# Optimization experiments

Hardware: AMD Instinct MI355X
Metric: run time of the kernel (lower is better)

Reference implementation:

```python
import jax, jax.numpy as jnp
import numpy as np
from jax import lax

# Module dims (match init_kwargs / input_specs)
CIN, COUT, K, STRIDE = 8, 16, 3, 2
U = V = 32                      # input spatial size (inshape = (CIN, U, V))
UO = VO = U // STRIDE           # 'same' padding with stride -> 16
IN_DIM = CIN * U * V + 1        # 8193 (homogeneous)
OUT_DIM = COUT * UO * VO + 1    # 4097 (homogeneous)
N = 1024                        # batch (columns of x_affine)


def setup_inputs() -> dict:
    key = jax.random.key(0)
    k1, k2, k3, k4, k5 = jax.random.split(key, 5)
    w = jax.random.normal(k1, (COUT, CIN, K, K), dtype=jnp.float32) * 0.1
    b = jax.random.normal(k2, (COUT,), dtype=jnp.float32) * 0.1
    # Keying matrices (dense stand-ins for the sparse keys); scaled to keep values sane.
    A = jax.random.normal(k3, (OUT_DIM, OUT_DIM), dtype=jnp.float32) / np.sqrt(OUT_DIM)
    Ainv = jax.random.normal(k4, (IN_DIM, IN_DIM), dtype=jnp.float32) / np.sqrt(IN_DIM)
    x_affine = jax.random.normal(k5, (IN_DIM, N), dtype=jnp.float32)
    return {"w": w, "b": b, "A": A, "Ainv": Ainv, "x_affine": x_affine}


def _toeplitz_conv_apply(z, w, b):
    """Apply the affine Toeplitz conv matrix T to z of shape (CIN*U*V+1, N).
    T = [[conv, bias], [0, 1]] so T@z = [conv(z[:-1]) + b*z[-1]; z[-1]]."""
    n = z.shape[1]
    hom = z[-1]                                   # (N,) homogeneous row
    x = z[:-1].T.reshape(n, CIN, U, V)            # (N, CIN, U, V)
    y = lax.conv_general_dilated(
        x, w, window_strides=(STRIDE, STRIDE), padding="SAME",
        dimension_numbers=("NCHW", "OIHW", "NCHW"))  # (N, COUT, UO, VO)
    y = y + b[None, :, None, None] * hom[:, None, None, None]
    yf = y.reshape(n, COUT * UO * VO).T           # (COUT*UO*VO, N)
    return jnp.concatenate([yf, hom[None, :]], axis=0)  # (OUT_DIM, N)


def reference(w, b, A, Ainv, x_affine):
    # What @ x = A @ T @ Ainv @ x  (factored; never materializes What)
    z = Ainv @ x_affine                # (IN_DIM, N)
    t = _toeplitz_conv_apply(z, w, b)  # (OUT_DIM, N)
    return A @ t                       # (OUT_DIM, N)
```

## Files before the change

kernel.cpp:

```cpp
#include <hip/hip_runtime.h>

#define IN_DIM 8193
#define OUT_DIM 4097
#define NB 1024
#define MP1 8448
#define KP1 8256
#define MP2 4352
#define KP2 4160

typedef __attribute__((ext_vector_type(8))) short short8;
typedef __attribute__((ext_vector_type(4))) float f32x4;

__device__ __forceinline__ unsigned short f2bf(float f) {
  unsigned int u = __float_as_uint(f);
  u = (u + 0x7fffu + ((u >> 16) & 1u)) >> 16;
  return (unsigned short)u;
}

__global__ __launch_bounds__(256) void cvt_pad_kernel(
    const float* __restrict__ src, unsigned short* __restrict__ dst,
    int sR, int sC, int dR, int dC) {
  int gid = blockIdx.x * 256 + threadIdx.x;
  int i4 = gid * 4;
  if (i4 >= dR * dC) return;
  int r = i4 / dC;
  int c = i4 - r * dC;
  unsigned short o[4];
#pragma unroll
  for (int j = 0; j < 4; ++j) {
    int cc = c + j;
    float v = (r < sR && cc < sC) ? src[(size_t)r * sC + cc] : 0.f;
    o[j] = f2bf(v);
  }
  unsigned int lo = (unsigned)o[0] | ((unsigned)o[1] << 16);
  unsigned int hi = (unsigned)o[2] | ((unsigned)o[3] << 16);
  *reinterpret_cast<uint2*>(dst + i4) = make_uint2(lo, hi);
}

__global__ __launch_bounds__(256) void transpose_cvt_kernel(
    const float* __restrict__ src, unsigned short* __restrict__ dst,
    int K, int N, int Kp) {
  __shared__ float tl[32][33];
  const int ntk = Kp >> 5;
  int bx = blockIdx.x % ntk;
  int by = blockIdx.x / ntk;
  int k0 = bx * 32, n0 = by * 32;
  int tx = threadIdx.x & 31, ty = threadIdx.x >> 5;
#pragma unroll
  for (int i = 0; i < 4; ++i) {
    int k = k0 + ty + i * 8;
    tl[ty + i * 8][tx] = (k < K) ? src[(size_t)k * N + n0 + tx] : 0.f;
  }
  __syncthreads();
#pragma unroll
  for (int i = 0; i < 4; ++i) {
    int n = n0 + ty + i * 8;
    dst[(size_t)n * Kp + k0 + tx] = f2bf(tl[tx][ty + i * 8]);
  }
}

__global__ __launch_bounds__(256) void zero_kernel(float4* __restrict__ p, int n) {
  int i = blockIdx.x * 256 + threadIdx.x;
  if (i < n) p[i] = make_float4(0.f, 0.f, 0.f, 0.f);
}

template <int NKT>
__global__ __launch_bounds__(512) void gemm_sk(
    const unsigned short* __restrict__ Ab,
    const unsigned short* __restrict__ Bt,
    float* __restrict__ C,
    int Kp, int Mout, int total_units) {
  extern __shared__ unsigned short lds[];
  const int tid = threadIdx.x;
  const int wid = tid >> 6;
  const int lane = tid & 63;
  const int wm = (wid >> 2) << 7;
  const int wn = (wid & 3) << 6;
  const int b = blockIdx.x;
  const int bw = ((b & 7) << 5) | (b >> 3);
  const int s = (int)(((long long)bw * total_units) >> 8);
  const int e = (int)(((long long)(bw + 1) * total_units) >> 8);

  const int g0 = ((lane >> 4) ^ (lane & 7)) * 8;
  const int g1 = ((4 + (lane >> 4)) ^ (lane & 7)) * 8;
  const int alo = (lane & 15) * 64;
  const int bhalf = (wn >> 7) << 1;
  const int ahalf = (wid >> 2) << 1;
  const int bsub = ((wn & 64) << 6) + alo;

#define STAGE(UNIT, ISA)                                                       \
  do {                                                                         \
    const int rq_ = (UNIT);                                                    \
    const int us_ = rq_ < e - 1 ? rq_ : e - 1;                                 \
    const int par_ = rq_ & 1;                                                  \
    const int tau_ = us_ / NKT;                                                \
    const int kt_ = us_ - tau_ * NKT;                                          \
    const size_t gr_ = (size_t)((ISA) ? (tau_ >> 2) : (tau_ & 3)) << 8;        \
    const unsigned short* M_ = (ISA) ? Ab : Bt;                                \
    _Pragma("unroll")                                                          \
    for (int h_ = 0; h_ < 2; ++h_) {                                           \
      _Pragma("unroll")                                                        \
      for (int L_ = 0; L_ < 2; ++L_) {                                         \
        const int s_ = L_ * 512 + tid;                                         \
        const int row_ = s_ >> 3;                                              \
        const int gl_ = (s_ & 7) ^ (row_ & 7);                                 \
        const unsigned short* g_ = M_ + (gr_ + (h_ << 7) + row_) * (size_t)Kp  \
                                      + (kt_ << 6) + gl_ * 8;                  \
        unsigned short* l_ = lds + (((ISA) ? 0 : 4) + (h_ << 1) + par_) * 8192 \
                                 + (size_t)(L_ * 512 + wid * 64) * 8;          \
        __builtin_amdgcn_global_load_lds(                                      \
            (const __attribute__((address_space(1))) void*)g_,                 \
            (__attribute__((address_space(3))) void*)l_, 16, 0, 0);            \
      }                                                                        \
    }                                                                          \
  } while (0)

#define MFMA16(BV0, BV1, NF0, NF1)                                             \
  do {                                                                         \
    __builtin_amdgcn_s_setprio(1);                                             \
    _Pragma("unroll")                                                          \
    for (int mf_ = 0; mf_ < 8; ++mf_) {                                        \
      asm volatile("v_mfma_f32_16x16x32_bf16 %0, %1, %2, %0"                   \
                   : "+v"(acc[mf_][NF0]) : "v"(af[mf_]), "v"(BV0));            \
      asm volatile("v_mfma_f32_16x16x32_bf16 %0, %1, %2, %0"                   \
                   : "+v"(acc[mf_][NF1]) : "v"(af[mf_]), "v"(BV1));            \
    }                                                                          \
    __builtin_amdgcn_s_setprio(0);                                             \
  } while (0)

#define FLUSH(TAU)                                                             \
  do {                                                                         \
    const int bm_ = (TAU) >> 2, bn_ = (TAU) & 3;                               \
    _Pragma("unroll")                                                          \
    for (int mf_ = 0; mf_ < 8; ++mf_) {                                        \
      const int rb_ = (bm_ << 8) + wm + mf_ * 16 + ((lane >> 4) << 2);         \
      _Pragma("unroll")                                                        \
      for (int nf_ = 0; nf_ < 4; ++nf_) {                                      \
        const int col_ = (bn_ << 8) + wn + nf_ * 16 + (lane & 15);             \
        _Pragma("unroll")                                                      \
        for (int r_ = 0; r_ < 4; ++r_) {                                       \
          const int row_ = rb_ + r_;                                           \
          if (row_ < Mout)                                                     \
            unsafeAtomicAdd(&C[(size_t)row_ * NB + col_], acc[mf_][nf_][r_]);  \
        }                                                                      \
        acc[mf_][nf_] = (f32x4)(0.0f);                                         \
      }                                                                        \
    }                                                                          \
  } while (0)

  f32x4 acc[8][4];
#pragma unroll
  for (int i = 0; i < 8; ++i)
#pragma unroll
    for (int j = 0; j < 4; ++j) acc[i][j] = (f32x4)(0.0f);

  STAGE(s, 1);
  STAGE(s, 0);
  STAGE(s + 1, 1);

  int tau_cur = s / NKT;
  for (int u = s; u < e; ++u) {
    const int par = u & 1;
    const unsigned short* Ab_ = lds + (ahalf + par) * 8192 + alo;
    const unsigned short* Bb_ = lds + (4 + bhalf + par) * 8192 + bsub;
    short8 af[8], b0, b1;
    __builtin_amdgcn_sched_barrier(0);
    asm volatile("s_waitcnt vmcnt(4)" ::: "memory");
    __builtin_amdgcn_s_barrier();
    __builtin_amdgcn_sched_barrier(0);
    STAGE(u + 1, 0);
#pragma unroll
    for (int mf = 0; mf < 8; ++mf)
      af[mf] = *reinterpret_cast<const short8*>(Ab_ + mf * 1024 + g0);
    b0 = *reinterpret_cast<const short8*>(Bb_ + 0 * 1024 + g0);
    b1 = *reinterpret_cast<const short8*>(Bb_ + 1 * 1024 + g0);
    MFMA16(b0, b1, 0, 1);
    b0 = *reinterpret_cast<const short8*>(Bb_ + 2 * 1024 + g0);
    b1 = *reinterpret_cast<const short8*>(Bb_ + 3 * 1024 + g0);
    MFMA16(b0, b1, 2, 3);
#pragma unroll
    for (int mf = 0; mf < 8; ++mf)
      af[mf] = *reinterpret_cast<const short8*>(Ab_ + mf * 1024 + g1);
    b0 = *reinterpret_cast<const short8*>(Bb_ + 2 * 1024 + g1);
    b1 = *reinterpret_cast<const short8*>(Bb_ + 3 * 1024 + g1);
    MFMA16(b0, b1, 2, 3);
    __builtin_amdgcn_sched_barrier(0);
    __builtin_amdgcn_s_barrier();
    __builtin_amdgcn_sched_barrier(0);
    STAGE(u + 2, 1);
    b0 = *reinterpret_cast<const short8*>(Bb_ + 0 * 1024 + g1);
    b1 = *reinterpret_cast<const short8*>(Bb_ + 1 * 1024 + g1);
    MFMA16(b0, b1, 0, 1);
    if (u + 1 >= e) {
      FLUSH(tau_cur);
    } else {
      const int tn = (u + 1) / NKT;
      if (tn != tau_cur) { FLUSH(tau_cur); tau_cur = tn; }
    }
  }
#undef STAGE
#undef MFMA16
#undef FLUSH
}

__global__ __launch_bounds__(256) void conv_tT_kernel(
    const float* __restrict__ z, const float* __restrict__ w,
    const float* __restrict__ bias, unsigned short* __restrict__ tT) {
  const int gid = blockIdx.x * 256 + threadIdx.x;
  const int n = gid & 1023;
  const int rg = gid >> 10;
  const int r0 = rg << 3;
  const float hom = z[(size_t)8192 * 1024 + n];
  unsigned short o[8];
  if (r0 >= 4096) {
#pragma unroll
    for (int j = 0; j < 8; ++j) o[j] = f2bf((r0 + j == 4096) ? hom : 0.f);
  } else {
    const int co = r0 >> 8;
    const int uo = (r0 >> 4) & 15;
    const int vo0 = r0 & 15;
    float acc[8];
    const float bb = bias[co];
#pragma unroll
    for (int j = 0; j < 8; ++j) acc[j] = bb * hom;
    for (int ci = 0; ci < 8; ++ci) {
#pragma unroll
      for (int kh = 0; kh < 3; ++kh) {
        const int u = uo * 2 + kh;
        if (u >= 32) continue;
        const float* zbase = z + (size_t)(ci * 1024 + u * 32) * 1024 + n;
#pragma unroll
        for (int kw = 0; kw < 3; ++kw) {
          const float wv = w[((co * 8 + ci) * 3 + kh) * 3 + kw];
#pragma unroll
          for (int j = 0; j < 8; ++j) {
            const int v = (vo0 + j) * 2 + kw;
            if (v < 32) acc[j] += wv * zbase[(size_t)v * 1024];
          }
        }
      }
    }
#pragma unroll
    for (int j = 0; j < 8; ++j) o[j] = f2bf(acc[j]);
  }
  uint4 pv;
  pv.x = (unsigned)o[0] | ((unsigned)o[1] << 16);
  pv.y = (unsigned)o[2] | ((unsigned)o[3] << 16);
  pv.z = (unsigned)o[4] | ((unsigned)o[5] << 16);
  pv.w = (unsigned)o[6] | ((unsigned)o[7] << 16);
  *reinterpret_cast<uint4*>(tT + (size_t)n * KP2 + r0) = pv;
}

extern "C" void kernel_launch(void* const* d_in, const int* in_sizes, int n_in,
                              void* d_out, int out_size, void* d_ws, size_t ws_size,
                              hipStream_t stream) {
  const float* w    = (const float*)d_in[0];
  const float* bias = (const float*)d_in[1];
  const float* A    = (const float*)d_in[2];
  const float* Ainv = (const float*)d_in[3];
  const float* x    = (const float*)d_in[4];
  float* out = (float*)d_out;

  char* ws = (char*)d_ws;
  unsigned short* Ainv_b = (unsigned short*)ws;
  unsigned short* xT_b   = (unsigned short*)(ws + (size_t)MP1 * KP1 * 2);
  float*          z      = (float*)(ws + (size_t)MP1 * KP1 * 2 + (size_t)NB * KP1 * 2);
  unsigned short* tT_b   = (unsigned short*)(ws + (size_t)MP1 * KP1 * 2 + (size_t)NB * KP1 * 2
                                             + (size_t)MP1 * NB * 4);
  unsigned short* A2_b   = Ainv_b;
  (void)ws_size; (void)in_sizes; (void)n_in; (void)out_size;

  hipFuncSetAttribute((const void*)gemm_sk<129>,
                      hipFuncAttributeMaxDynamicSharedMemorySize, 131072);
  hipFuncSetAttribute((const void*)gemm_sk<65>,
                      hipFuncAttributeMaxDynamicSharedMemorySize, 131072);

  cvt_pad_kernel<<<(MP1 * KP1 / 4 + 255) / 256, 256, 0, stream>>>(
      Ainv, Ainv_b, IN_DIM, IN_DIM, MP1, KP1);
  transpose_cvt_kernel<<<(KP1 / 32) * (NB / 32), 256, 0, stream>>>(
      x, xT_b, IN_DIM, NB, KP1);
  zero_kernel<<<(MP1 * NB / 4 + 255) / 256, 256, 0, stream>>>(
      (float4*)z, MP1 * NB / 4);
  gemm_sk<129><<<256, 512, 131072, stream>>>(
      Ainv_b, xT_b, z, KP1, MP1, 33 * 4 * 129);
  conv_tT_kernel<<<(520 * 1024) / 256, 256, 0, stream>>>(z, w, bias, tT_b);
  cvt_pad_kernel<<<(MP2 * KP2 / 4 + 255) / 256, 256, 0, stream>>>(
      A, A2_b, OUT_DIM, OUT_DIM, MP2, KP2);
  zero_kernel<<<(OUT_DIM * NB / 4 + 255) / 256, 256, 0, stream>>>(
      (float4*)out, OUT_DIM * NB / 4);
  gemm_sk<65><<<256, 512, 131072, stream>>>(
      A2_b, tT_b, out, KP2, OUT_DIM, 17 * 4 * 65);
}
```

Measured before the change: 439.8 us.

## Replace stream-K atomic GEMMs with fixed split-K partial buffers plus reductions

Both GEMMs move from stream-K scheduling with atomic flushes to a fixed data-parallel tiling over the unpadded 8192/4096 rows, with a static K split into separate partial buffers. The partials are reduced afterwards: the first GEMM's two halves are summed inside the conv kernel, and the second GEMM's four halves by a new sum kernel. The odd homogeneous rows are handled apart: the z row is a dot product fused into the transpose kernel, and the last output row comes from a small GEMV kernel. This removes the atomics, the zeroing passes and the padded-row work, at the cost of extra partial-buffer traffic and fp32 reduction passes.

```diff
diff --git a/kernel.cpp b/kernel.cpp
--- a/kernel.cpp
+++ b/kernel.cpp
@@ -3,9 +3,9 @@
 #define IN_DIM 8193
 #define OUT_DIM 4097
 #define NB 1024
-#define MP1 8448
+#define M1 8192
 #define KP1 8256
-#define MP2 4352
+#define M2 4096
 #define KP2 4160
 
 typedef __attribute__((ext_vector_type(8))) short short8;
@@ -15,6 +15,9 @@
   unsigned int u = __float_as_uint(f);
   u = (u + 0x7fffu + ((u >> 16) & 1u)) >> 16;
   return (unsigned short)u;
+}
+__device__ __forceinline__ float bf2f(unsigned short u) {
+  return __uint_as_float(((unsigned int)u) << 16);
 }
 
 __global__ __launch_bounds__(256) void cvt_pad_kernel(
@@ -37,8 +40,9 @@
   *reinterpret_cast<uint2*>(dst + i4) = make_uint2(lo, hi);
 }
 
-__global__ __launch_bounds__(256) void transpose_cvt_kernel(
+__global__ __launch_bounds__(256) void transpose_cvt_zh_kernel(
     const float* __restrict__ src, unsigned short* __restrict__ dst,
+    const float* __restrict__ arow, float* __restrict__ zh,
     int K, int N, int Kp) {
   __shared__ float tl[32][33];
   const int ntk = Kp >> 5;
@@ -51,11 +55,17 @@
     int k = k0 + ty + i * 8;
     tl[ty + i * 8][tx] = (k < K) ? src[(size_t)k * N + n0 + tx] : 0.f;
   }
+  const float av = (k0 + tx < K) ? arow[k0 + tx] : 0.f;
   __syncthreads();
 #pragma unroll
   for (int i = 0; i < 4; ++i) {
     int n = n0 + ty + i * 8;
-    dst[(size_t)n * Kp + k0 + tx] = f2bf(tl[tx][ty + i * 8]);
+    float v = tl[tx][ty + i * 8];
+    dst[(size_t)n * Kp + k0 + tx] = f2bf(v);
+    float c = av * v;
+#pragma unroll
+    for (int m = 1; m <= 16; m <<= 1) c += __shfl_xor(c, m);
+    if (tx == 0) atomicAdd(&zh[n], c);
   }
 }
 
@@ -64,22 +74,27 @@
   if (i < n) p[i] = make_float4(0.f, 0.f, 0.f, 0.f);
 }
 
-template <int NKT>
-__global__ __launch_bounds__(512) void gemm_sk(
+template <int NKT, int NSPLIT, int BMBITS, int MROWS>
+__global__ __launch_bounds__(512) void gemm_dp(
     const unsigned short* __restrict__ Ab,
     const unsigned short* __restrict__ Bt,
-    float* __restrict__ C,
-    int Kp, int Mout, int total_units) {
+    float* __restrict__ C, int Kp) {
   extern __shared__ unsigned short lds[];
   const int tid = threadIdx.x;
   const int wid = tid >> 6;
   const int lane = tid & 63;
+  const int b = blockIdx.x;
+  const int x = b & 7, q = b >> 3;
+  const int bm = (q & ((1 << BMBITS) - 1)) * 8 + x;
+  const int bn = (q >> BMBITS) & 3;
+  const int sp = q >> (BMBITS + 2);
   const int wm = (wid >> 2) << 7;
   const int wn = (wid & 3) << 6;
-  const int b = blockIdx.x;
-  const int bw = ((b & 7) << 5) | (b >> 3);
-  const int s = (int)(((long long)bw * total_units) >> 8);
-  const int e = (int)(((long long)(bw + 1) * total_units) >> 8);
+
+  const int qk = NKT / NSPLIT, rrk = NKT % NSPLIT;
+  const int kt0 = sp * qk + (sp < rrk ? sp : rrk);
+  const int T = qk + (sp < rrk ? 1 : 0);
+  float* Cp = C + (size_t)sp * MROWS * NB;
 
   const int g0 = ((lane >> 4) ^ (lane & 7)) * 8;
   const int g1 = ((4 + (lane >> 4)) ^ (lane & 7)) * 8;
@@ -88,15 +103,13 @@
   const int ahalf = (wid >> 2) << 1;
   const int bsub = ((wn & 64) << 6) + alo;
 
-#define STAGE(UNIT, ISA)                                                       \
+#define STAGE(TT, ISA)                                                         \
   do {                                                                         \
-    const int rq_ = (UNIT);                                                    \
-    const int us_ = rq_ < e - 1 ? rq_ : e - 1;                                 \
-    const int par_ = rq_ & 1;                                                  \
-    const int tau_ = us_ / NKT;                                                \
-    const int kt_ = us_ - tau_ * NKT;                                          \
-    const size_t gr_ = (size_t)((ISA) ? (tau_ >> 2) : (tau_ & 3)) << 8;        \
+    const int tt_ = (TT);                                                      \
+    const int kc_ = kt0 + (tt_ < T - 1 ? tt_ : T - 1);                         \
+    const int par_ = tt_ & 1;                                                  \
     const unsigned short* M_ = (ISA) ? Ab : Bt;                                \
+    const int br_ = ((ISA) ? bm : bn) << 8;                                    \
     _Pragma("unroll")                                                          \
     for (int h_ = 0; h_ < 2; ++h_) {                                           \
       _Pragma("unroll")                                                        \
@@ -104,8 +117,8 @@
         const int s_ = L_ * 512 + tid;                                         \
         const int row_ = s_ >> 3;                                              \
         const int gl_ = (s_ & 7) ^ (row_ & 7);                                 \
-        const unsigned short* g_ = M_ + (gr_ + (h_ << 7) + row_) * (size_t)Kp  \
-                                      + (kt_ << 6) + gl_ * 8;                  \
+        const unsigned short* g_ = M_ + (size_t)(br_ + (h_ << 7) + row_) * Kp  \
+                                      + (kc_ << 6) + gl_ * 8;                  \
         unsigned short* l_ = lds + (((ISA) ? 0 : 4) + (h_ << 1) + par_) * 8192 \
                                  + (size_t)(L_ * 512 + wid * 64) * 8;          \
         __builtin_amdgcn_global_load_lds(                                      \
@@ -128,39 +141,18 @@
     __builtin_amdgcn_s_setprio(0);                                             \
   } while (0)
 
-#define FLUSH(TAU)                                                             \
-  do {                                                                         \
-    const int bm_ = (TAU) >> 2, bn_ = (TAU) & 3;                               \
-    _Pragma("unroll")                                                          \
-    for (int mf_ = 0; mf_ < 8; ++mf_) {                                        \
-      const int rb_ = (bm_ << 8) + wm + mf_ * 16 + ((lane >> 4) << 2);         \
-      _Pragma("unroll")                                                        \
-      for (int nf_ = 0; nf_ < 4; ++nf_) {                                      \
-        const int col_ = (bn_ << 8) + wn + nf_ * 16 + (lane & 15);             \
-        _Pragma("unroll")                                                      \
-        for (int r_ = 0; r_ < 4; ++r_) {                                       \
-          const int row_ = rb_ + r_;                                           \
-          if (row_ < Mout)                                                     \
-            unsafeAtomicAdd(&C[(size_t)row_ * NB + col_], acc[mf_][nf_][r_]);  \
-        }                                                                      \
-        acc[mf_][nf_] = (f32x4)(0.0f);                                         \
-      }                                                                        \
-    }                                                                          \
-  } while (0)
-
   f32x4 acc[8][4];
 #pragma unroll
   for (int i = 0; i < 8; ++i)
 #pragma unroll
     for (int j = 0; j < 4; ++j) acc[i][j] = (f32x4)(0.0f);
 
-  STAGE(s, 1);
-  STAGE(s, 0);
-  STAGE(s + 1, 1);
-
-  int tau_cur = s / NKT;
-  for (int u = s; u < e; ++u) {
-    const int par = u & 1;
+  STAGE(0, 1);
+  STAGE(0, 0);
+  STAGE(1, 1);
+
+  for (int t = 0; t < T; ++t) {
+    const int par = t & 1;
     const unsigned short* Ab_ = lds + (ahalf + par) * 8192 + alo;
     const unsigned short* Bb_ = lds + (4 + bhalf + par) * 8192 + bsub;
     short8 af[8], b0, b1;
@@ -168,7 +160,7 @@
     asm volatile("s_waitcnt vmcnt(4)" ::: "memory");
     __builtin_amdgcn_s_barrier();
     __builtin_amdgcn_sched_barrier(0);
-    STAGE(u + 1, 0);
+    STAGE(t + 1, 0);
 #pragma unroll
     for (int mf = 0; mf < 8; ++mf)
       af[mf] = *reinterpret_cast<const short8*>(Ab_ + mf * 1024 + g0);
@@ -187,30 +179,36 @@
     __builtin_amdgcn_sched_barrier(0);
     __builtin_amdgcn_s_barrier();
     __builtin_amdgcn_sched_barrier(0);
-    STAGE(u + 2, 1);
+    STAGE(t + 2, 1);
     b0 = *reinterpret_cast<const short8*>(Bb_ + 0 * 1024 + g1);
     b1 = *reinterpret_cast<const short8*>(Bb_ + 1 * 1024 + g1);
     MFMA16(b0, b1, 0, 1);
-    if (u + 1 >= e) {
-      FLUSH(tau_cur);
-    } else {
-      const int tn = (u + 1) / NKT;
-      if (tn != tau_cur) { FLUSH(tau_cur); tau_cur = tn; }
-    }
   }
 #undef STAGE
 #undef MFMA16
-#undef FLUSH
+
+#pragma unroll
+  for (int mf = 0; mf < 8; ++mf) {
+    const int rb = (bm << 8) + wm + mf * 16 + ((lane >> 4) << 2);
+#pragma unroll
+    for (int nf = 0; nf < 4; ++nf) {
+      const int col = (bn << 8) + wn + nf * 16 + (lane & 15);
+#pragma unroll
+      for (int r = 0; r < 4; ++r)
+        Cp[(size_t)(rb + r) * NB + col] = acc[mf][nf][r];
+    }
+  }
 }
 
 __global__ __launch_bounds__(256) void conv_tT_kernel(
-    const float* __restrict__ z, const float* __restrict__ w,
+    const float* __restrict__ za, const float* __restrict__ zb,
+    const float* __restrict__ zh, const float* __restrict__ w,
     const float* __restrict__ bias, unsigned short* __restrict__ tT) {
   const int gid = blockIdx.x * 256 + threadIdx.x;
   const int n = gid & 1023;
   const int rg = gid >> 10;
   const int r0 = rg << 3;
-  const float hom = z[(size_t)8192 * 1024 + n];
+  const float hom = zh[n];
   unsigned short o[8];
   if (r0 >= 4096) {
 #pragma unroll
@@ -228,14 +226,17 @@
       for (int kh = 0; kh < 3; ++kh) {
         const int u = uo * 2 + kh;
         if (u >= 32) continue;
-        const float* zbase = z + (size_t)(ci * 1024 + u * 32) * 1024 + n;
+        const size_t zoff = (size_t)(ci * 1024 + u * 32) * 1024 + n;
 #pragma unroll
         for (int kw = 0; kw < 3; ++kw) {
           const float wv = w[((co * 8 + ci) * 3 + kh) * 3 + kw];
 #pragma unroll
           for (int j = 0; j < 8; ++j) {
             const int v = (vo0 + j) * 2 + kw;
-            if (v < 32) acc[j] += wv * zbase[(size_t)v * 1024];
+            if (v < 32) {
+              const size_t e = zoff + (size_t)v * 1024;
+              acc[j] += wv * (za[e] + zb[e]);
+            }
           }
         }
       }
@@ -249,6 +250,47 @@
   pv.z = (unsigned)o[4] | ((unsigned)o[5] << 16);
   pv.w = (unsigned)o[6] | ((unsigned)o[7] << 16);
   *reinterpret_cast<uint4*>(tT + (size_t)n * KP2 + r0) = pv;
+}
+
+__global__ __launch_bounds__(256) void sum4_kernel(
+    const float* __restrict__ p, float* __restrict__ out, int n4) {
+  const int i = blockIdx.x * 256 + threadIdx.x;
+  if (i >= n4) return;
+  const size_t stride4 = (size_t)M2 * NB / 4;
+  const float4* p4 = (const float4*)p;
+  float4 a = p4[i];
+  float4 b = p4[i + stride4];
+  float4 c = p4[i + 2 * stride4];
+  float4 d = p4[i + 3 * stride4];
+  float4 r;
+  r.x = (a.x + b.x) + (c.x + d.x);
+  r.y = (a.y + b.y) + (c.y + d.y);
+  r.z = (a.z + b.z) + (c.z + d.z);
+  r.w = (a.w + b.w) + (c.w + d.w);
+  reinterpret_cast<float4*>(out)[i] = r;
+}
+
+__global__ __launch_bounds__(256) void outrow_kernel(
+    const unsigned short* __restrict__ A2row,
+    const unsigned short* __restrict__ tT, float* __restrict__ out) {
+  const int wid = threadIdx.x >> 6, lane = threadIdx.x & 63;
+  const int n = blockIdx.x * 4 + wid;
+  const unsigned short* trow = tT + (size_t)n * KP2;
+  float acc = 0.f;
+#pragma unroll
+  for (int it = 0; it < 9; ++it) {
+    const int i8 = it * 64 + lane;
+    if (i8 < KP2 / 8) {
+      short8 tv = *reinterpret_cast<const short8*>(trow + i8 * 8);
+      short8 av = *reinterpret_cast<const short8*>(A2row + i8 * 8);
+#pragma unroll
+      for (int j = 0; j < 8; ++j)
+        acc += bf2f((unsigned short)tv[j]) * bf2f((unsigned short)av[j]);
+    }
+  }
+#pragma unroll
+  for (int m = 1; m <= 32; m <<= 1) acc += __shfl_xor(acc, m);
+  if (lane == 0) out[(size_t)4096 * NB + n] = acc;
 }
 
 extern "C" void kernel_launch(void* const* d_in, const int* in_sizes, int n_in,
@@ -262,32 +304,39 @@
   float* out = (float*)d_out;
 
   char* ws = (char*)d_ws;
+  const size_t o_xT = (size_t)M1 * KP1 * 2;
+  const size_t o_z2 = o_xT + (size_t)NB * KP1 * 2;
+  const size_t o_tT = o_z2 + (size_t)2 * M1 * NB * 4;
+  const size_t o_zh = o_tT + (size_t)NB * KP2 * 2;
   unsigned short* Ainv_b = (unsigned short*)ws;
-  unsigned short* xT_b   = (unsigned short*)(ws + (size_t)MP1 * KP1 * 2);
-  float*          z      = (float*)(ws + (size_t)MP1 * KP1 * 2 + (size_t)NB * KP1 * 2);
-  unsigned short* tT_b   = (unsigned short*)(ws + (size_t)MP1 * KP1 * 2 + (size_t)NB * KP1 * 2
-                                             + (size_t)MP1 * NB * 4);
-  unsigned short* A2_b   = Ainv_b;
+  unsigned short* xT_b   = (unsigned short*)(ws + o_xT);
+  float*          z2     = (float*)(ws + o_z2);
+  unsigned short* tT_b   = (unsigned short*)(ws + o_tT);
+  float*          zh     = (float*)(ws + o_zh);
+  unsigned short* A2_b   = (unsigned short*)ws;
+  float*          outp   = (float*)(ws + (size_t)OUT_DIM * KP2 * 2);
   (void)ws_size; (void)in_sizes; (void)n_in; (void)out_size;
 
-  hipFuncSetAttribute((const void*)gemm_sk<129>,
+  hipFuncSetAttribute((const void*)gemm_dp<129, 2, 2, M1>,
                       hipFuncAttributeMaxDynamicSharedMemorySize, 131072);
-  hipFuncSetAttribute((const void*)gemm_sk<65>,
+  hipFuncSetAttribute((const void*)gemm_dp<65, 4, 1, M2>,
                       hipFuncAttributeMaxDynamicSharedMemorySize, 131072);
 
-  cvt_pad_kernel<<<(MP1 * KP1 / 4 + 255) / 256, 256, 0, stream>>>(
-      Ainv, Ainv_b, IN_DIM, IN_DIM, MP1, KP1);
-  transpose_cvt_kernel<<<(KP1 / 32) * (NB / 32), 256, 0, stream>>>(
-      x, xT_b, IN_DIM, NB, KP1);
-  zero_kernel<<<(MP1 * NB / 4 + 255) / 256, 256, 0, stream>>>(
-      (float4*)z, MP1 * NB / 4);
-  gemm_sk<129><<<256, 512, 131072, stream>>>(
-      Ainv_b, xT_b, z, KP1, MP1, 33 * 4 * 129);
-  conv_tT_kernel<<<(520 * 1024) / 256, 256, 0, stream>>>(z, w, bias, tT_b);
-  cvt_pad_kernel<<<(MP2 * KP2 / 4 + 255) / 256, 256, 0, stream>>>(
-      A, A2_b, OUT_DIM, OUT_DIM, MP2, KP2);
-  zero_kernel<<<(OUT_DIM * NB / 4 + 255) / 256, 256, 0, stream>>>(
-      (float4*)out, OUT_DIM * NB / 4);
-  gemm_sk<65><<<256, 512, 131072, stream>>>(
-      A2_b, tT_b, out, KP2, OUT_DIM, 17 * 4 * 65);
-}
+  zero_kernel<<<1, 256, 0, stream>>>((float4*)zh, 256);
+  cvt_pad_kernel<<<(M1 * KP1 / 4) / 256, 256, 0, stream>>>(
+      Ainv, Ainv_b, IN_DIM, IN_DIM, M1, KP1);
+  transpose_cvt_zh_kernel<<<(KP1 / 32) * (NB / 32), 256, 0, stream>>>(
+      x, xT_b, Ainv + (size_t)8192 * IN_DIM, zh, IN_DIM, NB, KP1);
+  gemm_dp<129, 2, 2, M1><<<256, 512, 131072, stream>>>(
+      Ainv_b, xT_b, z2, KP1);
+  conv_tT_kernel<<<(520 * 1024) / 256, 256, 0, stream>>>(
+      z2, z2 + (size_t)M1 * NB, zh, w, bias, tT_b);
+  cvt_pad_kernel<<<(OUT_DIM * KP2 / 4 + 255) / 256, 256, 0, stream>>>(
+      A, A2_b, OUT_DIM, OUT_DIM, OUT_DIM, KP2);
+  gemm_dp<65, 4, 1, M2><<<256, 512, 131072, stream>>>(
+      A2_b, tT_b, outp, KP2);
+  sum4_kernel<<<(M2 * NB / 4) / 256, 256, 0, stream>>>(
+      outp, out, M2 * NB / 4);
+  outrow_kernel<<<NB / 4, 256, 0, stream>>>(
+      A2_b + (size_t)4096 * KP2, tT_b, out);
+}
```

New measurement: 569.2 us. 1.29x slower.
